# Kernel tuning notes

Hardware: AMD Instinct MI355X
Metric: run time of the kernel (lower is better)

Reference implementation:

```python
import jax, jax.numpy as jnp
import numpy as np

B, S, D = 2, 2048, 1024
H = 16
DK = D // H
FF = 4096
EPS = 1e-6


def setup_inputs() -> dict:
    key = jax.random.key(0)
    ks = jax.random.split(key, 16)
    sd = 0.02
    inp = {
        "x": jax.random.normal(ks[0], (B, S, D), dtype=jnp.float32),
        # attention projections (stored as [in, out]; y = x @ W + b)
        "Wq": jax.random.normal(ks[1], (D, D), dtype=jnp.float32) * sd,
        "bq": jnp.zeros((D,), jnp.float32),
        "Wk": jax.random.normal(ks[2], (D, D), dtype=jnp.float32) * sd,
        "bk": jnp.zeros((D,), jnp.float32),
        "Wv": jax.random.normal(ks[3], (D, D), dtype=jnp.float32) * sd,
        "bv": jnp.zeros((D,), jnp.float32),
        "Wo": jax.random.normal(ks[4], (D, D), dtype=jnp.float32) * sd,
        "bo": jnp.zeros((D,), jnp.float32),
        # FFN
        "W1": jax.random.normal(ks[5], (D, FF), dtype=jnp.float32) * sd,
        "b1": jnp.zeros((FF,), jnp.float32),
        "W2": jax.random.normal(ks[6], (FF, D), dtype=jnp.float32) * sd,
        "b2": jnp.zeros((D,), jnp.float32),
        # LayerNorms (pre-norm)
        "ln1_g": jnp.ones((D,), jnp.float32),
        "ln1_b": jnp.zeros((D,), jnp.float32),
        "ln2_g": jnp.ones((D,), jnp.float32),
        "ln2_b": jnp.zeros((D,), jnp.float32),
    }
    return inp


def _layer_norm(x, g, b):
    mu = jnp.mean(x, axis=-1, keepdims=True)
    var = jnp.mean(jnp.square(x - mu), axis=-1, keepdims=True)
    return (x - mu) * jax.lax.rsqrt(var + EPS) * g + b


def _attention(x, Wq, bq, Wk, bk, Wv, bv, Wo, bo):
    # project and split heads: [B,S,D] -> [B,H,S,DK]
    def split(t):
        return t.reshape(B, S, H, DK).transpose(0, 2, 1, 3)
    q = split(x @ Wq + bq)
    k = split(x @ Wk + bk)
    v = split(x @ Wv + bv)
    scores = jnp.einsum("bhqd,bhkd->bhqk", q, k) / jnp.sqrt(jnp.float32(DK))
    p = jax.nn.softmax(scores, axis=-1)  # no mask in forward path; dropout eval-mode
    o = jnp.einsum("bhqk,bhkd->bhqd", p, v)
    o = o.transpose(0, 2, 1, 3).reshape(B, S, D)
    return o @ Wo + bo


def reference(x, Wq, bq, Wk, bk, Wv, bv, Wo, bo, W1, b1, W2, b2,
              ln1_g, ln1_b, ln2_g, ln2_b):
    # sublayer 1: x + attn(LN(x))
    x = x + _attention(_layer_norm(x, ln1_g, ln1_b), Wq, bq, Wk, bk, Wv, bv, Wo, bo)
    # sublayer 2: x + FFN(LN(x))
    h = jax.nn.relu(_layer_norm(x, ln2_g, ln2_b) @ W1 + b1)
    x = x + (h @ W2 + b2)
    return x
```

## Files before the change

kernel.cpp:

```cpp
#include <hip/hip_runtime.h>


#define S_LEN 2048
#define DMODEL 1024
#define NHEADS 16
#define FFDIM 4096
#define MROWS 4096

typedef _Float16 f16;
typedef _Float16 f16x8 __attribute__((ext_vector_type(8)));
typedef __fp16 fp16x2 __attribute__((ext_vector_type(2)));
typedef float f32x4 __attribute__((ext_vector_type(4)));
typedef unsigned int u32;
typedef unsigned long long u64;
typedef unsigned long long u64x2 __attribute__((ext_vector_type(2)));

union Frag { f16x8 h; u64 q[2]; f16 e[8]; u32 w[4]; };

__device__ __forceinline__ f32x4 mfma16(f16x8 a, f16x8 b, f32x4 c) {
  return __builtin_amdgcn_mfma_f32_16x16x32_f16(a, b, c, 0, 0, 0);
}

__device__ __forceinline__ u32 pk16(float lo, float hi) {
  fp16x2 v = __builtin_amdgcn_cvt_pkrtz(lo, hi);
  return __builtin_bit_cast(u32, v);
}

typedef __attribute__((address_space(1))) const void gvoid;
typedef __attribute__((address_space(3))) void lvoid;

__device__ __forceinline__ void gload16(const f16* gp, f16* lp) {
  __builtin_amdgcn_global_load_lds((gvoid*)gp, (lvoid*)lp, 16, 0, 0);
}

__global__ __launch_bounds__(256) void wtrans_kernel(const float* __restrict__ W,
                                                     f16* __restrict__ Wt,
                                                     int K, int N) {
  __shared__ f16 tile[32][33];
  const int n0 = blockIdx.x * 32, k0 = blockIdx.y * 32;
  const int tx = threadIdx.x & 31, ty = threadIdx.x >> 5;
  for (int i = 0; i < 4; i++) {
    int k = ty + i * 8;
    tile[k][tx] = (f16)W[(size_t)(k0 + k) * N + n0 + tx];
  }
  __syncthreads();
  for (int i = 0; i < 4; i++) {
    int n = ty + i * 8;
    Wt[(size_t)(n0 + n) * K + k0 + tx] = tile[tx][n];
  }
}

__global__ __launch_bounds__(256) void wtrans4_kernel(const float* __restrict__ W0,
                                                      const float* __restrict__ W1,
                                                      const float* __restrict__ W2,
                                                      const float* __restrict__ W3,
                                                      f16* __restrict__ D0,
                                                      f16* __restrict__ D1,
                                                      f16* __restrict__ D2,
                                                      f16* __restrict__ D3) {
  const int z = blockIdx.z;
  const float* W = z == 0 ? W0 : z == 1 ? W1 : z == 2 ? W2 : W3;
  f16* Wt = z == 0 ? D0 : z == 1 ? D1 : z == 2 ? D2 : D3;
  __shared__ f16 tile[32][33];
  const int n0 = blockIdx.x * 32, k0 = blockIdx.y * 32;
  const int tx = threadIdx.x & 31, ty = threadIdx.x >> 5;
  for (int i = 0; i < 4; i++) {
    int k = ty + i * 8;
    tile[k][tx] = (f16)W[(size_t)(k0 + k) * 1024 + n0 + tx];
  }
  __syncthreads();
  for (int i = 0; i < 4; i++) {
    int n = ty + i * 8;
    Wt[(size_t)(n0 + n) * 1024 + k0 + tx] = tile[tx][n];
  }
}

__global__ void bias_concat_kernel(const float* __restrict__ bq,
                                   const float* __restrict__ bk,
                                   const float* __restrict__ bv,
                                   float* __restrict__ out) {
  int i = blockIdx.x * 256 + threadIdx.x;
  float v = (i < 1024) ? bq[i] : (i < 2048) ? bk[i - 1024] : bv[i - 2048];
  out[i] = v;
}

__global__ __launch_bounds__(256) void ln_kernel(const float* __restrict__ x,
                                                 const float* __restrict__ gw,
                                                 const float* __restrict__ bw,
                                                 f16* __restrict__ out) {
  const int row = blockIdx.x, t = threadIdx.x;
  const float* xr = x + (size_t)row * DMODEL;
  float4 v = *(const float4*)(xr + t * 4);
  float s = v.x + v.y + v.z + v.w;
  float s2 = v.x * v.x + v.y * v.y + v.z * v.z + v.w * v.w;
  for (int off = 1; off < 64; off <<= 1) {
    s += __shfl_xor(s, off);
    s2 += __shfl_xor(s2, off);
  }
  __shared__ float red[8];
  const int w = t >> 6, lane = t & 63;
  if (lane == 0) { red[w] = s; red[w + 4] = s2; }
  __syncthreads();
  s = red[0] + red[1] + red[2] + red[3];
  s2 = red[4] + red[5] + red[6] + red[7];
  float mu = s * (1.0f / DMODEL);
  float var = s2 * (1.0f / DMODEL) - mu * mu;
  float rstd = rsqrtf(var + 1e-6f);
  float4 g4 = *(const float4*)(gw + t * 4);
  float4 b4 = *(const float4*)(bw + t * 4);
  union { f16 h[4]; u64 q; } o;
  o.h[0] = (f16)((v.x - mu) * rstd * g4.x + b4.x);
  o.h[1] = (f16)((v.y - mu) * rstd * g4.y + b4.y);
  o.h[2] = (f16)((v.z - mu) * rstd * g4.z + b4.z);
  o.h[3] = (f16)((v.w - mu) * rstd * g4.w + b4.w);
  *(u64*)(out + (size_t)row * DMODEL + t * 4) = o.q;
}

template <int BM, int BN>
__global__ __launch_bounds__(256, 2) void gemm2(const f16* __restrict__ A, int lda,
                                                const f16* __restrict__ Bt, int ldb,
                                                const float* __restrict__ bias,
                                                const float* __restrict__ res,
                                                float* __restrict__ outf,
                                                f16* __restrict__ outh, int ldo,
                                                int N, int K, int relu) {
  constexpr int MT = BM / 32, NT = BN / 32;
  __shared__ f16 As[2][BM * 64];
  __shared__ f16 Bs[2][BN * 64];
  const int gx = gridDim.x;
  const int nwg = gx * gridDim.y;
  int id = blockIdx.y * gx + blockIdx.x;
  id = (id & 7) * (nwg >> 3) + (id >> 3);
  const int m0 = (id / gx) * BM, n0 = (id % gx) * BN;
  const int t = threadIdx.x;
  const int lane = t & 63, w = t >> 6;
  const int wr = w >> 1, wc = w & 1;
  const int rA = lane & 15, g = lane >> 4;

  f32x4 acc[MT][NT] = {};

  auto stageA = [&](int k0, int buf) {
#pragma unroll
    for (int p = 0; p < BM / 32; p++) {
      const int chunk = p * 256 + w * 64 + lane;
      const int row = chunk >> 3;
      const int cbg = ((chunk & 7) ^ (row & 7)) * 8;
      gload16(A + (size_t)(m0 + row) * lda + k0 + cbg,
              &As[buf][(p * 256 + w * 64) * 8]);
    }
  };
  auto stageB = [&](int k0, int buf) {
#pragma unroll
    for (int p = 0; p < BN / 32; p++) {
      const int chunk = p * 256 + w * 64 + lane;
      const int row = chunk >> 3;
      const int cbg = ((chunk & 7) ^ (row & 7)) * 8;
      gload16(Bt + (size_t)(n0 + row) * ldb + k0 + cbg,
              &Bs[buf][(p * 256 + w * 64) * 8]);
    }
  };

  auto compute = [&](int cur) {
#pragma unroll
    for (int ks = 0; ks < 2; ks++) {
      Frag a[MT], b[NT];
#pragma unroll
      for (int mt = 0; mt < MT; mt++) {
        const int row = wr * (BM / 2) + mt * 16 + rA;
        a[mt].h = *(const f16x8*)(&As[cur][row * 64 + ((ks * 4 + g) ^ (row & 7)) * 8]);
      }
#pragma unroll
      for (int nt = 0; nt < NT; nt++) {
        const int row = wc * (BN / 2) + nt * 16 + rA;
        b[nt].h = *(const f16x8*)(&Bs[cur][row * 64 + ((ks * 4 + g) ^ (row & 7)) * 8]);
      }
#pragma unroll
      for (int mt = 0; mt < MT; mt++)
#pragma unroll
        for (int nt = 0; nt < NT; nt++)
          acc[mt][nt] = mfma16(a[mt].h, b[nt].h, acc[mt][nt]);
    }
  };

  const int nsteps = K / 64;
  stageA(0, 0);
  stageB(0, 0);
  stageA(64, 1);

  for (int ts = 0; ts < nsteps - 1; ++ts) {
    const int cur = ts & 1;
    asm volatile("s_waitcnt vmcnt(4)" ::: "memory");
    __builtin_amdgcn_sched_barrier(0);
    __builtin_amdgcn_s_barrier();
    stageB(ts * 64 + 64, cur ^ 1);
    compute(cur);
    asm volatile("s_waitcnt lgkmcnt(0)" ::: "memory");
    __builtin_amdgcn_sched_barrier(0);
    __builtin_amdgcn_s_barrier();
    if (ts + 2 < nsteps) stageA(ts * 64 + 128, cur);
  }
  asm volatile("s_waitcnt vmcnt(0)" ::: "memory");
  __builtin_amdgcn_sched_barrier(0);
  __builtin_amdgcn_s_barrier();
  compute((nsteps - 1) & 1);

#pragma unroll
  for (int mt = 0; mt < MT; mt++) {
#pragma unroll
    for (int nt = 0; nt < NT; nt++) {
      const int col = n0 + wc * (BN / 2) + nt * 16 + rA;
      const int rowb = m0 + wr * (BM / 2) + mt * 16 + g * 4;
      const float bs = bias[col];
#pragma unroll
      for (int r = 0; r < 4; r++) {
        float v = acc[mt][nt][r] + bs;
        if (relu) v = fmaxf(v, 0.0f);
        if (res) v += res[(size_t)(rowb + r) * N + col];
        if (outf) outf[(size_t)(rowb + r) * N + col] = v;
        if (outh) outh[(size_t)(rowb + r) * ldo + col] = (f16)v;
      }
    }
  }
}

__global__ __launch_bounds__(256) void vtrans_kernel(const f16* __restrict__ qkv,
                                                     f16* __restrict__ vt) {
  const int bh = blockIdx.y;
  const int s0 = blockIdx.x * 64;
  const int b = bh >> 4, h = bh & 15;
  __shared__ f16 tile[64][72];
  const int t = threadIdx.x;
  for (int pass = 0; pass < 2; pass++) {
    int sl = (t >> 3) + pass * 32;
    int dk0 = (t & 7) * 8;
    u64x2 v = *(const u64x2*)(qkv + (size_t)(b * S_LEN + s0 + sl) * 3072 + 2048 + h * 64 + dk0);
    *(u64x2*)(&tile[sl][dk0]) = v;
  }
  __syncthreads();
  for (int pass = 0; pass < 2; pass++) {
    int dk = (t >> 3) + pass * 32;
    int sc = (t & 7) * 8;
    union { u64x2 q; f16 u[8]; } o;
    for (int j = 0; j < 8; j++) {
      int pos = sc + j;
      int kv = (pos & 32) | ((pos & 4) << 2) | ((pos & 0x18) >> 1) | (pos & 3);
      o.u[j] = tile[kv][dk];
    }
    *(u64x2*)(vt + (size_t)(bh * 64 + dk) * S_LEN + s0 + sc) = o.q;
  }
}

__global__ __launch_bounds__(256, 4) void attn_kernel(const f16* __restrict__ qkv,
                                                      const f16* __restrict__ vt,
                                                      f16* __restrict__ attn_out) {
  const int qt0 = blockIdx.x * 64;
  const int bh = blockIdx.y;
  const int b = bh >> 4, h = bh & 15;
  const int t = threadIdx.x;
  const int lane = t & 63, w = t >> 6;
  const int rA = lane & 15, g = lane >> 4;

  __shared__ f16 Ks[2][64 * 64];
  __shared__ f16 Vs[2][64 * 64];

  const int qrow = qt0 + w * 16 + rA;
  Frag qf[2];
#pragma unroll
  for (int kt = 0; kt < 2; kt++) {
    const f16* p = qkv + (size_t)(b * S_LEN + qrow) * 3072 + h * 64 + kt * 32 + 8 * g;
    f16x8 v = *(const f16x8*)p;
#pragma unroll
    for (int j = 0; j < 8; j++) v[j] = v[j] * (f16)0.18033688f;
    qf[kt].h = v;
  }

  float lR = 0.0f;
  f32x4 o2[4] = {};

#define STAGE_KV(kv0_, buf_)                                                     \
  {                                                                              \
    _Pragma("unroll") for (int i = 0; i < 2; i++) {                              \
      int C = i * 256 + w * 64 + lane;                                           \
      int row = C >> 3;                                                          \
      int cbg = ((C & 7) ^ (row & 7)) * 8;                                       \
      gload16(qkv + (size_t)(b * S_LEN + (kv0_) + row) * 3072 + 1024 + h * 64 + cbg, \
              &Ks[buf_][(i * 256 + w * 64) * 8]);                                \
      gload16(vt + (size_t)(bh * 64 + row) * S_LEN + (kv0_) + cbg,               \
              &Vs[buf_][(i * 256 + w * 64) * 8]);                                \
    }                                                                            \
  }

  int cur = 0;
  STAGE_KV(0, 0);

  for (int kv0 = 0; kv0 < S_LEN; kv0 += 64) {
    __syncthreads();
    if (kv0 + 64 < S_LEN) STAGE_KV(kv0 + 64, cur ^ 1);

    f32x4 s[4] = {};
#pragma unroll
    for (int nt = 0; nt < 4; nt++) {
      const int row = nt * 16 + rA;
#pragma unroll
      for (int kt = 0; kt < 2; kt++) {
        Frag kf;
        kf.h = *(const f16x8*)(&Ks[cur][row * 64 + ((kt * 4 + g) ^ (row & 7)) * 8]);
        s[nt] = mfma16(kf.h, qf[kt].h, s[nt]);
      }
    }

    float rs = 0.0f;
#pragma unroll
    for (int nt = 0; nt < 4; nt++)
#pragma unroll
      for (int r = 0; r < 4; r++) {
        float e0 = exp2f(s[nt][r]);
        s[nt][r] = e0;
        rs += e0;
      }
    rs += __shfl_xor(rs, 16);
    rs += __shfl_xor(rs, 32);
    lR += rs;

    Frag ph[2];
#pragma unroll
    for (int j = 0; j < 2; j++) {
      ph[j].w[0] = pk16(s[2 * j][0], s[2 * j][1]);
      ph[j].w[1] = pk16(s[2 * j][2], s[2 * j][3]);
      ph[j].w[2] = pk16(s[2 * j + 1][0], s[2 * j + 1][1]);
      ph[j].w[3] = pk16(s[2 * j + 1][2], s[2 * j + 1][3]);
    }

#pragma unroll
    for (int ntd = 0; ntd < 4; ntd++) {
      const int row = ntd * 16 + rA;
#pragma unroll
      for (int j = 0; j < 2; j++) {
        Frag vf;
        vf.h = *(const f16x8*)(&Vs[cur][row * 64 + ((j * 4 + g) ^ (row & 7)) * 8]);
        o2[ntd] = mfma16(vf.h, ph[j].h, o2[ntd]);
      }
    }

    cur ^= 1;
  }

  const float inv = 1.0f / lR;
#pragma unroll
  for (int ntd = 0; ntd < 4; ntd++) {
    union { f16 h[4]; u64 q; } pk;
#pragma unroll
    for (int r = 0; r < 4; r++) pk.h[r] = (f16)(o2[ntd][r] * inv);
    *(u64*)(attn_out + (size_t)(b * S_LEN + qrow) * DMODEL + h * 64 + ntd * 16 + g * 4) = pk.q;
  }
#undef STAGE_KV
}

extern "C" void kernel_launch(void* const* d_in, const int* in_sizes, int n_in,
                              void* d_out, int out_size, void* d_ws, size_t ws_size,
                              hipStream_t stream) {
  const float* x     = (const float*)d_in[0];
  const float* Wq    = (const float*)d_in[1];
  const float* bq    = (const float*)d_in[2];
  const float* Wk    = (const float*)d_in[3];
  const float* bk    = (const float*)d_in[4];
  const float* Wv    = (const float*)d_in[5];
  const float* bv    = (const float*)d_in[6];
  const float* Wo    = (const float*)d_in[7];
  const float* bo    = (const float*)d_in[8];
  const float* W1    = (const float*)d_in[9];
  const float* b1    = (const float*)d_in[10];
  const float* W2    = (const float*)d_in[11];
  const float* b2    = (const float*)d_in[12];
  const float* ln1g  = (const float*)d_in[13];
  const float* ln1b  = (const float*)d_in[14];
  const float* ln2g  = (const float*)d_in[15];
  const float* ln2b  = (const float*)d_in[16];
  float* out = (float*)d_out;
  char* ws = (char*)d_ws;

  size_t off = 0;
  f16* wqkv_t = (f16*)(ws + off); off += (size_t)3072 * 1024 * 2;
  f16* wo_t   = (f16*)(ws + off); off += (size_t)1024 * 1024 * 2;
  f16* w1_t   = (f16*)(ws + off); off += (size_t)4096 * 1024 * 2;
  f16* w2_t   = (f16*)(ws + off); off += (size_t)1024 * 4096 * 2;
  float* bqkv = (float*)(ws + off); off += 3072 * 4;
  f16* regB   = (f16*)(ws + off); off += (size_t)MROWS * 1024 * 2;
  f16* qkv    = (f16*)(ws + off); off += (size_t)MROWS * 3072 * 2;
  f16* vt     = (f16*)(ws + off); off += (size_t)MROWS * 1024 * 2;
  f16* hbuf   = qkv;

  wtrans4_kernel<<<dim3(32, 32, 4), 256, 0, stream>>>(
      Wq, Wk, Wv, Wo,
      wqkv_t, wqkv_t + (size_t)1024 * 1024, wqkv_t + (size_t)2048 * 1024, wo_t);
  wtrans_kernel<<<dim3(128, 32), 256, 0, stream>>>(W1, w1_t, 1024, 4096);
  wtrans_kernel<<<dim3(32, 128), 256, 0, stream>>>(W2, w2_t, 4096, 1024);
  bias_concat_kernel<<<12, 256, 0, stream>>>(bq, bk, bv, bqkv);

  ln_kernel<<<MROWS, 256, 0, stream>>>(x, ln1g, ln1b, regB);

  gemm2<128, 128><<<dim3(24, 32), 256, 0, stream>>>(regB, 1024, wqkv_t, 1024, bqkv,
                                                    nullptr, nullptr, qkv, 3072,
                                                    3072, 1024, 0);
  vtrans_kernel<<<dim3(32, 32), 256, 0, stream>>>(qkv, vt);

  attn_kernel<<<dim3(32, 32), 256, 0, stream>>>(qkv, vt, regB);

  gemm2<128, 64><<<dim3(16, 32), 256, 0, stream>>>(regB, 1024, wo_t, 1024, bo,
                                                   x, out, nullptr, 0,
                                                   1024, 1024, 0);
  ln_kernel<<<MROWS, 256, 0, stream>>>(out, ln2g, ln2b, regB);

  gemm2<128, 128><<<dim3(32, 32), 256, 0, stream>>>(regB, 1024, w1_t, 1024, b1,
                                                    nullptr, nullptr, hbuf, 4096,
                                                    4096, 1024, 1);
  gemm2<128, 64><<<dim3(16, 32), 256, 0, stream>>>(hbuf, 4096, w2_t, 4096, b2,
                                                   out, out, nullptr, 0,
                                                   1024, 4096, 0);
}
```

Baseline: 281.5 us.

## Double attention query rows per block, merge weight transposes, widen QKV GEMM tile

The attention kernel now gives each wave 32 query rows, split into two 16-row groups, so every K and V fragment read from LDS feeds two MFMAs. The row-sum reduction moves out of the inner loop into the epilogue. This halves the attention grid and the K/V staging traffic per query, at the cost of more registers and lower occupancy (launch bounds drop to 2). Separately, the W1 and W2 transposes merge into one launch, and the QKV GEMM switches to a 128x192 tile with 16x32 blocks.

```diff
diff --git a/kernel.cpp b/kernel.cpp
--- a/kernel.cpp
+++ b/kernel.cpp
@@ -31,23 +31,6 @@
 
 __device__ __forceinline__ void gload16(const f16* gp, f16* lp) {
   __builtin_amdgcn_global_load_lds((gvoid*)gp, (lvoid*)lp, 16, 0, 0);
-}
-
-__global__ __launch_bounds__(256) void wtrans_kernel(const float* __restrict__ W,
-                                                     f16* __restrict__ Wt,
-                                                     int K, int N) {
-  __shared__ f16 tile[32][33];
-  const int n0 = blockIdx.x * 32, k0 = blockIdx.y * 32;
-  const int tx = threadIdx.x & 31, ty = threadIdx.x >> 5;
-  for (int i = 0; i < 4; i++) {
-    int k = ty + i * 8;
-    tile[k][tx] = (f16)W[(size_t)(k0 + k) * N + n0 + tx];
-  }
-  __syncthreads();
-  for (int i = 0; i < 4; i++) {
-    int n = ty + i * 8;
-    Wt[(size_t)(n0 + n) * K + k0 + tx] = tile[tx][n];
-  }
 }
 
 __global__ __launch_bounds__(256) void wtrans4_kernel(const float* __restrict__ W0,
@@ -72,6 +55,29 @@
   for (int i = 0; i < 4; i++) {
     int n = ty + i * 8;
     Wt[(size_t)(n0 + n) * 1024 + k0 + tx] = tile[tx][n];
+  }
+}
+
+__global__ __launch_bounds__(256) void wtrans2_kernel(const float* __restrict__ W1,
+                                                      const float* __restrict__ W2,
+                                                      f16* __restrict__ D1,
+                                                      f16* __restrict__ D2) {
+  const int z = blockIdx.z;
+  const float* W = z ? W2 : W1;
+  f16* Wt = z ? D2 : D1;
+  const int K = z ? 4096 : 1024, N = z ? 1024 : 4096;
+  const int n0 = (z ? blockIdx.y : blockIdx.x) * 32;
+  const int k0 = (z ? blockIdx.x : blockIdx.y) * 32;
+  __shared__ f16 tile[32][33];
+  const int tx = threadIdx.x & 31, ty = threadIdx.x >> 5;
+  for (int i = 0; i < 4; i++) {
+    int k = ty + i * 8;
+    tile[k][tx] = (f16)W[(size_t)(k0 + k) * N + n0 + tx];
+  }
+  __syncthreads();
+  for (int i = 0; i < 4; i++) {
+    int n = ty + i * 8;
+    Wt[(size_t)(n0 + n) * K + k0 + tx] = tile[tx][n];
   }
 }
 
@@ -250,10 +256,10 @@
   }
 }
 
-__global__ __launch_bounds__(256, 4) void attn_kernel(const f16* __restrict__ qkv,
+__global__ __launch_bounds__(256, 2) void attn_kernel(const f16* __restrict__ qkv,
                                                       const f16* __restrict__ vt,
                                                       f16* __restrict__ attn_out) {
-  const int qt0 = blockIdx.x * 64;
+  const int qt0 = blockIdx.x * 128;
   const int bh = blockIdx.y;
   const int b = bh >> 4, h = bh & 15;
   const int t = threadIdx.x;
@@ -263,19 +269,21 @@
   __shared__ f16 Ks[2][64 * 64];
   __shared__ f16 Vs[2][64 * 64];
 
-  const int qrow = qt0 + w * 16 + rA;
-  Frag qf[2];
-#pragma unroll
-  for (int kt = 0; kt < 2; kt++) {
-    const f16* p = qkv + (size_t)(b * S_LEN + qrow) * 3072 + h * 64 + kt * 32 + 8 * g;
-    f16x8 v = *(const f16x8*)p;
-#pragma unroll
-    for (int j = 0; j < 8; j++) v[j] = v[j] * (f16)0.18033688f;
-    qf[kt].h = v;
-  }
-
-  float lR = 0.0f;
-  f32x4 o2[4] = {};
+  Frag qf[2][2];
+#pragma unroll
+  for (int qg = 0; qg < 2; qg++)
+#pragma unroll
+    for (int kt = 0; kt < 2; kt++) {
+      const f16* p = qkv + (size_t)(b * S_LEN + qt0 + w * 32 + qg * 16 + rA) * 3072 +
+                     h * 64 + kt * 32 + 8 * g;
+      f16x8 v = *(const f16x8*)p;
+#pragma unroll
+      for (int j = 0; j < 8; j++) v[j] = v[j] * (f16)0.18033688f;
+      qf[qg][kt].h = v;
+    }
+
+  float lRp[2] = {0.0f, 0.0f};
+  f32x4 o2[2][4] = {};
 
 #define STAGE_KV(kv0_, buf_)                                                     \
   {                                                                              \
@@ -297,38 +305,43 @@
     __syncthreads();
     if (kv0 + 64 < S_LEN) STAGE_KV(kv0 + 64, cur ^ 1);
 
-    f32x4 s[4] = {};
-#pragma unroll
-    for (int nt = 0; nt < 4; nt++) {
-      const int row = nt * 16 + rA;
+    Frag kf[4][2];
+#pragma unroll
+    for (int nt = 0; nt < 4; nt++)
 #pragma unroll
       for (int kt = 0; kt < 2; kt++) {
-        Frag kf;
-        kf.h = *(const f16x8*)(&Ks[cur][row * 64 + ((kt * 4 + g) ^ (row & 7)) * 8]);
-        s[nt] = mfma16(kf.h, qf[kt].h, s[nt]);
-      }
-    }
-
-    float rs = 0.0f;
-#pragma unroll
-    for (int nt = 0; nt < 4; nt++)
-#pragma unroll
-      for (int r = 0; r < 4; r++) {
-        float e0 = exp2f(s[nt][r]);
-        s[nt][r] = e0;
-        rs += e0;
-      }
-    rs += __shfl_xor(rs, 16);
-    rs += __shfl_xor(rs, 32);
-    lR += rs;
-
-    Frag ph[2];
-#pragma unroll
-    for (int j = 0; j < 2; j++) {
-      ph[j].w[0] = pk16(s[2 * j][0], s[2 * j][1]);
-      ph[j].w[1] = pk16(s[2 * j][2], s[2 * j][3]);
-      ph[j].w[2] = pk16(s[2 * j + 1][0], s[2 * j + 1][1]);
-      ph[j].w[3] = pk16(s[2 * j + 1][2], s[2 * j + 1][3]);
+        const int row = nt * 16 + rA;
+        kf[nt][kt].h = *(const f16x8*)(&Ks[cur][row * 64 + ((kt * 4 + g) ^ (row & 7)) * 8]);
+      }
+    f32x4 s[2][4] = {};
+#pragma unroll
+    for (int qg = 0; qg < 2; qg++)
+#pragma unroll
+      for (int nt = 0; nt < 4; nt++)
+#pragma unroll
+        for (int kt = 0; kt < 2; kt++)
+          s[qg][nt] = mfma16(kf[nt][kt].h, qf[qg][kt].h, s[qg][nt]);
+
+    Frag ph[2][2];
+#pragma unroll
+    for (int qg = 0; qg < 2; qg++) {
+      float rs = 0.0f;
+#pragma unroll
+      for (int nt = 0; nt < 4; nt++)
+#pragma unroll
+        for (int r = 0; r < 4; r++) {
+          float e0 = exp2f(s[qg][nt][r]);
+          s[qg][nt][r] = e0;
+          rs += e0;
+        }
+      lRp[qg] += rs;
+#pragma unroll
+      for (int j = 0; j < 2; j++) {
+        ph[qg][j].w[0] = pk16(s[qg][2 * j][0], s[qg][2 * j][1]);
+        ph[qg][j].w[1] = pk16(s[qg][2 * j][2], s[qg][2 * j][3]);
+        ph[qg][j].w[2] = pk16(s[qg][2 * j + 1][0], s[qg][2 * j + 1][1]);
+        ph[qg][j].w[3] = pk16(s[qg][2 * j + 1][2], s[qg][2 * j + 1][3]);
+      }
     }
 
 #pragma unroll
@@ -338,20 +351,29 @@
       for (int j = 0; j < 2; j++) {
         Frag vf;
         vf.h = *(const f16x8*)(&Vs[cur][row * 64 + ((j * 4 + g) ^ (row & 7)) * 8]);
-        o2[ntd] = mfma16(vf.h, ph[j].h, o2[ntd]);
+#pragma unroll
+        for (int qg = 0; qg < 2; qg++)
+          o2[qg][ntd] = mfma16(vf.h, ph[qg][j].h, o2[qg][ntd]);
       }
     }
 
     cur ^= 1;
   }
 
-  const float inv = 1.0f / lR;
-#pragma unroll
-  for (int ntd = 0; ntd < 4; ntd++) {
-    union { f16 h[4]; u64 q; } pk;
-#pragma unroll
-    for (int r = 0; r < 4; r++) pk.h[r] = (f16)(o2[ntd][r] * inv);
-    *(u64*)(attn_out + (size_t)(b * S_LEN + qrow) * DMODEL + h * 64 + ntd * 16 + g * 4) = pk.q;
+#pragma unroll
+  for (int qg = 0; qg < 2; qg++) {
+    float l = lRp[qg];
+    l += __shfl_xor(l, 16);
+    l += __shfl_xor(l, 32);
+    const float inv = 1.0f / l;
+    const int qrow = qt0 + w * 32 + qg * 16 + rA;
+#pragma unroll
+    for (int ntd = 0; ntd < 4; ntd++) {
+      union { f16 h[4]; u64 q; } pk;
+#pragma unroll
+      for (int r = 0; r < 4; r++) pk.h[r] = (f16)(o2[qg][ntd][r] * inv);
+      *(u64*)(attn_out + (size_t)(b * S_LEN + qrow) * DMODEL + h * 64 + ntd * 16 + g * 4) = pk.q;
+    }
   }
 #undef STAGE_KV
 }
@@ -393,18 +415,17 @@
   wtrans4_kernel<<<dim3(32, 32, 4), 256, 0, stream>>>(
       Wq, Wk, Wv, Wo,
       wqkv_t, wqkv_t + (size_t)1024 * 1024, wqkv_t + (size_t)2048 * 1024, wo_t);
-  wtrans_kernel<<<dim3(128, 32), 256, 0, stream>>>(W1, w1_t, 1024, 4096);
-  wtrans_kernel<<<dim3(32, 128), 256, 0, stream>>>(W2, w2_t, 4096, 1024);
+  wtrans2_kernel<<<dim3(128, 32, 2), 256, 0, stream>>>(W1, W2, w1_t, w2_t);
   bias_concat_kernel<<<12, 256, 0, stream>>>(bq, bk, bv, bqkv);
 
   ln_kernel<<<MROWS, 256, 0, stream>>>(x, ln1g, ln1b, regB);
 
-  gemm2<128, 128><<<dim3(24, 32), 256, 0, stream>>>(regB, 1024, wqkv_t, 1024, bqkv,
+  gemm2<128, 192><<<dim3(16, 32), 256, 0, stream>>>(regB, 1024, wqkv_t, 1024, bqkv,
                                                     nullptr, nullptr, qkv, 3072,
                                                     3072, 1024, 0);
   vtrans_kernel<<<dim3(32, 32), 256, 0, stream>>>(qkv, vt);
 
-  attn_kernel<<<dim3(32, 32), 256, 0, stream>>>(qkv, vt, regB);
+  attn_kernel<<<dim3(16, 32), 256, 0, stream>>>(qkv, vt, regB);
 
   gemm2<128, 64><<<dim3(16, 32), 256, 0, stream>>>(regB, 1024, wo_t, 1024, bo,
                                                    x, out, nullptr, 0,
```

Measured after the change: 270.3 us. 1.04x faster.
